# Kernel tuning notes

Hardware: AMD Instinct MI355X
Metric: run time of the kernel (lower is better)

Reference implementation:

```python
import jax, jax.numpy as jnp
import numpy as np

IMG = 1536
STRIDES = [8, 16, 32, 64, 128]
SCALES = np.array([2.0 ** 0, 2.0 ** (1.0 / 3.0), 2.0 ** (2.0 / 3.0)])
RATIOS = np.array([0.5, 1.0, 2.0])
THRESHOLD = 0.5
IOU_THRESHOLD = 0.5
N_KEEP = 1000  # fixed candidate budget for jit-compatible NMS


def make_anchors():
    """Multi-level RetinaNet-style anchors in (x1, y1, x2, y2), [A, 4]."""
    all_boxes = []
    for s in STRIDES:
        base = 4.0 * s
        fs = IMG // s
        areas = (base * SCALES) ** 2
        ws, hs = [], []
        for r in RATIOS:
            ws.append(np.sqrt(areas / r))
            hs.append(np.sqrt(areas * r))
        ws = np.concatenate(ws)  # [9]
        hs = np.concatenate(hs)
        cx = (np.arange(fs) + 0.5) * s
        cy = (np.arange(fs) + 0.5) * s
        cxg, cyg = np.meshgrid(cx, cy)
        cxg = cxg.reshape(-1, 1)
        cyg = cyg.reshape(-1, 1)
        boxes = np.stack([cxg - ws / 2, cyg - hs / 2, cxg + ws / 2, cyg + hs / 2], axis=-1)
        all_boxes.append(boxes.reshape(-1, 4))
    return np.concatenate(all_boxes, axis=0).astype(np.float32)


def setup_inputs() -> dict:
    key = jax.random.key(0)
    k1, k2 = jax.random.split(key)
    anchors = jnp.asarray(make_anchors())  # [441936, 4]
    A = anchors.shape[0]
    cla = jax.random.uniform(k1, (1, A, 80), dtype=jnp.float32)  # sigmoid-like class scores
    reg = 0.1 * jax.random.normal(k2, (1, A, 4), dtype=jnp.float32)  # box deltas
    return {"cla": cla, "reg": reg, "anchors": anchors, "height": IMG, "width": IMG}


def decode_box(anchors, deltas):
    wa = anchors[:, 2] - anchors[:, 0]
    ha = anchors[:, 3] - anchors[:, 1]
    cxa = anchors[:, 0] + 0.5 * wa
    cya = anchors[:, 1] + 0.5 * ha
    cx = cxa + deltas[:, 0] * wa
    cy = cya + deltas[:, 1] * ha
    w = wa * jnp.exp(deltas[:, 2])
    h = ha * jnp.exp(deltas[:, 3])
    return jnp.stack([cx - 0.5 * w, cy - 0.5 * h, cx + 0.5 * w, cy + 0.5 * h], axis=-1)


def iou_matrix(b):
    x1 = jnp.maximum(b[:, None, 0], b[None, :, 0])
    y1 = jnp.maximum(b[:, None, 1], b[None, :, 1])
    x2 = jnp.minimum(b[:, None, 2], b[None, :, 2])
    y2 = jnp.minimum(b[:, None, 3], b[None, :, 3])
    inter = jnp.clip(x2 - x1, 0.0) * jnp.clip(y2 - y1, 0.0)
    area = jnp.clip(b[:, 2] - b[:, 0], 0.0) * jnp.clip(b[:, 3] - b[:, 1], 0.0)
    union = area[:, None] + area[None, :] - inter
    return inter / jnp.maximum(union, 1e-8)


def reference(cla, reg, anchors, height, width):
    # decode + clip (clipbox)
    boxes = decode_box(anchors, reg[0])  # [A, 4]
    boxes = jnp.stack([
        jnp.clip(boxes[:, 0], 0.0, width - 1.0),
        jnp.clip(boxes[:, 1], 0.0, height - 1.0),
        jnp.clip(boxes[:, 2], 0.0, width - 1.0),
        jnp.clip(boxes[:, 3], 0.0, height - 1.0),
    ], axis=-1)
    # per-anchor best class score (torch.max over dim=2)
    scores_all = jnp.max(cla[0], axis=1)  # [A]
    # fixed-size candidate set replaces data-dependent boolean masking
    top_scores, idx = jax.lax.top_k(scores_all, N_KEEP)
    cand_boxes = boxes[idx]            # [N, 4]
    cand_cla = cla[0][idx]             # [N, C]
    valid = top_scores > THRESHOLD     # score thresholding
    iou = iou_matrix(cand_boxes)       # [N, N]

    def body(i, keep):
        suppressed = jnp.any(keep & (iou[i] > IOU_THRESHOLD))
        return keep.at[i].set(valid[i] & ~suppressed)

    keep = jax.lax.fori_loop(0, N_KEEP, body, jnp.zeros((N_KEEP,), dtype=bool))

    nms_scores = jnp.where(keep, jnp.max(cand_cla, axis=1), 0.0)
    nms_class = jnp.where(keep, jnp.argmax(cand_cla, axis=1), -1)
    nms_boxes = jnp.where(keep[:, None], cand_boxes, 0.0)
    return nms_scores, nms_class, nms_boxes
```

## Files before the change

### kernel.cpp

```cpp
#include <hip/hip_runtime.h>
#include <stdint.h>


#define NK 1000
#define CAP 2048
#define NCLS 80
#define NW 16
typedef unsigned long long ull;

static inline __device__ unsigned fkey(float f) {
  unsigned u = __float_as_uint(f);
  return (u & 0x80000000u) ? ~u : (u | 0x80000000u);
}
static inline __device__ float fkey_inv(unsigned k) {
  unsigned u = (k & 0x80000000u) ? (k & 0x7fffffffu) : ~k;
  return __uint_as_float(u);
}

__device__ __forceinline__ void scan_select(const unsigned* __restrict__ gh, int nbins,
                                            unsigned k, unsigned* s_sum, unsigned* s_res,
                                            unsigned& digit, unsigned& cum_above) {
  int t = threadIdx.x;
  int chunk = nbins >> 8;
  int base = t * chunk;
  unsigned s = 0;
  for (int b = 0; b < chunk; ++b) s += gh[base + b];
  s_sum[t] = s;
  __syncthreads();
  unsigned ca = 0;
  for (int u = t + 1; u < 256; ++u) ca += s_sum[u];
  if (ca < k && ca + s >= k) {
    unsigned cum = ca;
    for (int b = chunk - 1; b >= 0; --b) {
      unsigned c = gh[base + b];
      if (cum + c >= k) { s_res[0] = (unsigned)(base + b); s_res[1] = cum; break; }
      cum += c;
    }
  }
  __syncthreads();
  digit = s_res[0];
  cum_above = s_res[1];
  __syncthreads();
}

__global__ __launch_bounds__(256) void k_score(const float* __restrict__ cla,
                                               unsigned* __restrict__ keys,
                                               unsigned* __restrict__ hist0, int A) {
  __shared__ unsigned lh[4096];
  int t = threadIdx.x;
  for (int i = t; i < 4096; i += 256) lh[i] = 0u;
  __syncthreads();
  const int lane = t & 63, wib = t >> 6;
  const int gwave = blockIdx.x * 4 + wib, nwaves = gridDim.x * 4;
  const int q = lane >> 2, sub = lane & 3;
  const int ntask = (A + 15) >> 4;
  for (int task = gwave; task < ntask; task += nwaves) {
    int a = task * 16 + q;
    float m = -3.402823466e38f;
    if (a < A) {
      const float4* p = (const float4*)(cla + (size_t)a * NCLS);
#pragma unroll
      for (int j = 0; j < 5; ++j) {
        float4 v = p[sub + j * 4];
        m = fmaxf(m, fmaxf(fmaxf(v.x, v.y), fmaxf(v.z, v.w)));
      }
    }
    m = fmaxf(m, __shfl_xor(m, 1, 64));
    m = fmaxf(m, __shfl_xor(m, 2, 64));
    if (sub == 0 && a < A) {
      unsigned key = fkey(m);
      keys[a] = key;
      atomicAdd(&lh[key >> 20], 1u);
    }
  }
  __syncthreads();
  for (int i = t; i < 4096; i += 256) {
    unsigned c = lh[i];
    if (c) atomicAdd(&hist0[i], c);
  }
}

__global__ __launch_bounds__(256) void k_hist1(const unsigned* __restrict__ keys,
                                               const unsigned* __restrict__ hist0,
                                               unsigned* __restrict__ hist1, int A) {
  __shared__ unsigned lh[4096];
  __shared__ unsigned s_sum[256];
  __shared__ unsigned s_res[2];
  int t = threadIdx.x;
  unsigned d0, ca;
  scan_select(hist0, 4096, NK, s_sum, s_res, d0, ca);
  for (int i = t; i < 4096; i += 256) lh[i] = 0u;
  __syncthreads();
  int tid = blockIdx.x * 256 + t, nthr = gridDim.x * 256;
  for (int a = tid; a < A; a += nthr) {
    unsigned key = keys[a];
    if ((key >> 20) == d0) atomicAdd(&lh[(key >> 8) & 0xFFFu], 1u);
  }
  __syncthreads();
  for (int i = t; i < 4096; i += 256) {
    unsigned c = lh[i];
    if (c) atomicAdd(&hist1[i], c);
  }
}

__global__ __launch_bounds__(256) void k_hist2(const unsigned* __restrict__ keys,
                                               const unsigned* __restrict__ hist0,
                                               const unsigned* __restrict__ hist1,
                                               unsigned* __restrict__ hist2, int A) {
  __shared__ unsigned lh[256];
  __shared__ unsigned s_sum[256];
  __shared__ unsigned s_res[2];
  int t = threadIdx.x;
  unsigned k_rem = NK, d0, d1, ca;
  scan_select(hist0, 4096, k_rem, s_sum, s_res, d0, ca);
  k_rem -= ca;
  scan_select(hist1, 4096, k_rem, s_sum, s_res, d1, ca);
  unsigned pref24 = (d0 << 12) | d1;
  lh[t] = 0u;
  __syncthreads();
  int tid = blockIdx.x * 256 + t, nthr = gridDim.x * 256;
  for (int a = tid; a < A; a += nthr) {
    unsigned key = keys[a];
    if ((key >> 8) == pref24) atomicAdd(&lh[key & 0xFFu], 1u);
  }
  __syncthreads();
  unsigned c = lh[t];
  if (c) atomicAdd(&hist2[t], c);
}

__global__ __launch_bounds__(256) void k_gather(const unsigned* __restrict__ keys,
                                                const unsigned* __restrict__ hist0,
                                                const unsigned* __restrict__ hist1,
                                                const unsigned* __restrict__ hist2,
                                                unsigned* __restrict__ cand_count,
                                                ull* __restrict__ cand_keys, int A) {
  __shared__ unsigned s_sum[256];
  __shared__ unsigned s_res[2];
  __shared__ ull lbuf[1024];
  __shared__ unsigned lcnt;
  __shared__ unsigned gbase;
  int t = threadIdx.x;
  unsigned k_rem = NK, d0, d1, d2, ca;
  scan_select(hist0, 4096, k_rem, s_sum, s_res, d0, ca);
  k_rem -= ca;
  scan_select(hist1, 4096, k_rem, s_sum, s_res, d1, ca);
  k_rem -= ca;
  scan_select(hist2, 256, k_rem, s_sum, s_res, d2, ca);
  const unsigned T = (((d0 << 12) | d1) << 8) | d2;
  if (t == 0) lcnt = 0u;
  __syncthreads();
  int tid = blockIdx.x * 256 + t, nthr = gridDim.x * 256;
  for (int a = tid; a < A; a += nthr) {
    unsigned key = keys[a];
    if (key >= T) {
      unsigned pos = atomicAdd(&lcnt, 1u);
      if (pos < 1024)
        lbuf[pos] = ((ull)key << 32) | (ull)(~(unsigned)a);
    }
  }
  __syncthreads();
  if (t == 0) gbase = (lcnt > 0) ? atomicAdd(cand_count, lcnt) : 0u;
  __syncthreads();
  unsigned n = lcnt < 1024u ? lcnt : 1024u;
  for (unsigned i = t; i < n; i += 256) {
    unsigned pos = gbase + i;
    if (pos < CAP) cand_keys[pos] = lbuf[i];
  }
}

__global__ __launch_bounds__(256) void k_rankdec(
    const float* __restrict__ cla, const float* __restrict__ reg,
    const float* __restrict__ anchors, const int* __restrict__ hp,
    const int* __restrict__ wp, const ull* __restrict__ cand_keys,
    float4* __restrict__ cand_box, float* __restrict__ cand_area,
    float* __restrict__ cand_score, int* __restrict__ cand_cls,
    int* __restrict__ cand_valid) {
  __shared__ ull skeys[CAP];
  int t = threadIdx.x;
  for (int i = t; i < CAP; i += 256) skeys[i] = cand_keys[i];
  __syncthreads();
  int c = blockIdx.x * 256 + t;
  ull ck = skeys[c];
  if (ck == 0ull) return;
  unsigned cnt = 0;
  const ulonglong2* sk2 = (const ulonglong2*)skeys;
#pragma unroll 4
  for (int j = 0; j < CAP / 2; ++j) {
    ulonglong2 v = sk2[j];
    cnt += (v.x > ck) ? 1u : 0u;
    cnt += (v.y > ck) ? 1u : 0u;
  }
  if (cnt >= NK) return;
  int rank = (int)cnt;
  unsigned a = ~(unsigned)(ck & 0xFFFFFFFFull);
  float score = fkey_inv((unsigned)(ck >> 32));
  float W1 = (float)wp[0] - 1.0f;
  float H1 = (float)hp[0] - 1.0f;
  float4 dd = ((const float4*)reg)[a];
  float4 an = ((const float4*)anchors)[a];
  float wa = an.z - an.x, ha = an.w - an.y;
  float cxa = an.x + 0.5f * wa, cya = an.y + 0.5f * ha;
  float cx = cxa + dd.x * wa, cy = cya + dd.y * ha;
  float w = wa * expf(dd.z), h = ha * expf(dd.w);
  float x1 = fminf(fmaxf(cx - 0.5f * w, 0.0f), W1);
  float y1 = fminf(fmaxf(cy - 0.5f * h, 0.0f), H1);
  float x2 = fminf(fmaxf(cx + 0.5f * w, 0.0f), W1);
  float y2 = fminf(fmaxf(cy + 0.5f * h, 0.0f), H1);
  cand_box[rank] = make_float4(x1, y1, x2, y2);
  cand_area[rank] = fmaxf(x2 - x1, 0.0f) * fmaxf(y2 - y1, 0.0f);
  cand_score[rank] = score;
  cand_valid[rank] = (score > 0.5f) ? 1 : 0;
  const float* row = cla + (size_t)a * NCLS;
  float m = -3.402823466e38f;
  int ci = 0;
#pragma unroll
  for (int j = 0; j < NCLS; ++j) {
    float v = row[j];
    if (v > m) { m = v; ci = j; }
  }
  cand_cls[rank] = ci;
}

__global__ __launch_bounds__(256) void k_supmat(const float4* __restrict__ cand_box,
                                                const float* __restrict__ cand_area,
                                                ull* __restrict__ sup) {
  __shared__ float4 bx[NK];
  __shared__ float ar[NK];
  int t = threadIdx.x;
  for (int i = t; i < NK; i += 256) {
    bx[i] = cand_box[i];
    ar[i] = cand_area[i];
  }
  __syncthreads();
  int g = blockIdx.x * 256 + t;
  int i = g >> 4, w = g & 15;
  if (i >= NK) return;
  float4 bi = bx[i];
  float ai = ar[i];
  ull bits = 0ull;
  int j0 = w * 64;
  int jend = (j0 + 64 < NK) ? (j0 + 64) : NK;
  for (int j = j0; j < jend; ++j) {
    float4 bj = bx[j];
    float xx1 = fmaxf(bi.x, bj.x), yy1 = fmaxf(bi.y, bj.y);
    float xx2 = fminf(bi.z, bj.z), yy2 = fminf(bi.w, bj.w);
    float inter = fmaxf(xx2 - xx1, 0.0f) * fmaxf(yy2 - yy1, 0.0f);
    float uni = ai + ar[j] - inter;
    float iou = inter / fmaxf(uni, 1e-8f);
    if (iou > 0.5f) bits |= (1ull << (j - j0));
  }
  sup[(size_t)i * NW + w] = bits;
}

__global__ __launch_bounds__(1024) void k_resolve(const ull* __restrict__ sup,
                                                  const int* __restrict__ cand_valid,
                                                  const float* __restrict__ cand_score,
                                                  const int* __restrict__ cand_cls,
                                                  const float4* __restrict__ cand_box,
                                                  float* __restrict__ out) {
  __shared__ ull keep_sh[NW];
  int t = threadIdx.x;
  if (t < 64) {
    int lane = t;
    ull keepw[NW];
#pragma unroll
    for (int c = 0; c < NW; ++c) {
      int row = c * 64 + lane;
      ull rw[NW];
      int vld = 0;
      if (row < NK) {
#pragma unroll
        for (int w = 0; w < NW; ++w) rw[w] = sup[(size_t)row * NW + w];
        vld = cand_valid[row];
      } else {
#pragma unroll
        for (int w = 0; w < NW; ++w) rw[w] = 0ull;
      }
      ull prev = 0ull;
#pragma unroll
      for (int w = 0; w < NW; ++w)
        if (w < c) prev |= rw[w] & keepw[w];
      int flags = (vld ? 2 : 0) | ((prev != 0ull) ? 1 : 0);
      unsigned Llo = (unsigned)rw[c];
      unsigned Lhi = (unsigned)(rw[c] >> 32);
      ull kept = 0ull;
      for (int b = 0; b < 64; ++b) {
        int fb = __shfl(flags, b, 64);
        unsigned lo = (unsigned)__shfl((int)Llo, b, 64);
        unsigned hi = (unsigned)__shfl((int)Lhi, b, 64);
        ull Lb = ((ull)hi << 32) | (ull)lo;
        bool kp = ((fb & 2) != 0) && ((fb & 1) == 0) && ((Lb & kept) == 0ull);
        kept |= ((ull)(kp ? 1u : 0u)) << b;
      }
      keepw[c] = kept;
    }
    if (lane == 0) {
#pragma unroll
      for (int w = 0; w < NW; ++w) keep_sh[w] = keepw[w];
    }
  }
  __syncthreads();
  for (int i = t; i < NK; i += 1024) {
    bool kp = (keep_sh[i >> 6] >> (i & 63)) & 1ull;
    out[i] = kp ? cand_score[i] : 0.0f;
    out[NK + i] = kp ? (float)cand_cls[i] : -1.0f;
    float4 b = cand_box[i];
    ((float4*)(out + 2 * NK))[i] = kp ? b : make_float4(0.f, 0.f, 0.f, 0.f);
  }
}

extern "C" void kernel_launch(void* const* d_in, const int* in_sizes, int n_in,
                              void* d_out, int out_size, void* d_ws, size_t ws_size,
                              hipStream_t stream) {
  const float* cla = (const float*)d_in[0];
  const float* reg = (const float*)d_in[1];
  const float* anchors = (const float*)d_in[2];
  const int* hp = (const int*)d_in[3];
  const int* wp = (const int*)d_in[4];
  float* out = (float*)d_out;
  int A = in_sizes[2] / 4;

  char* ws = (char*)d_ws;
  size_t off = 0;
  auto carve = [&](size_t bytes) -> void* {
    void* p = ws + off;
    off += bytes;
    off = (off + 255) & ~(size_t)255;
    return p;
  };
  unsigned* keys = (unsigned*)carve((size_t)A * 4);
  char* zbase = ws + off;
  unsigned* hist0 = (unsigned*)carve(4096 * 4);
  unsigned* hist1 = (unsigned*)carve(4096 * 4);
  unsigned* hist2 = (unsigned*)carve(256 * 4);
  unsigned* cand_count = (unsigned*)carve(4);
  ull* cand_keys = (ull*)carve(CAP * 8);
  size_t zbytes = (size_t)((ws + off) - zbase);
  float4* cand_box = (float4*)carve(1024 * 16);
  float* cand_area = (float*)carve(1024 * 4);
  float* cand_score = (float*)carve(1024 * 4);
  int* cand_cls = (int*)carve(1024 * 4);
  int* cand_valid = (int*)carve(1024 * 4);
  ull* sup = (ull*)carve((size_t)1024 * NW * 8);
  (void)ws_size;
  (void)n_in;
  (void)out_size;

  hipMemsetAsync(zbase, 0, zbytes, stream);
  k_score<<<1024, 256, 0, stream>>>(cla, keys, hist0, A);
  k_hist1<<<512, 256, 0, stream>>>(keys, hist0, hist1, A);
  k_hist2<<<512, 256, 0, stream>>>(keys, hist0, hist1, hist2, A);
  k_gather<<<512, 256, 0, stream>>>(keys, hist0, hist1, hist2, cand_count, cand_keys, A);
  k_rankdec<<<8, 256, 0, stream>>>(cla, reg, anchors, hp, wp, cand_keys, cand_box,
                                   cand_area, cand_score, cand_cls, cand_valid);
  k_supmat<<<63, 256, 0, stream>>>(cand_box, cand_area, sup);
  k_resolve<<<1, 1024, 0, stream>>>(sup, cand_valid, cand_score, cand_cls, cand_box, out);
}
```

Baseline: 359.2 us.

## Merge radix-select passes via 20-bit leaf histogram and fuse suppression with resolve

```diff
diff --git a/kernel.cpp b/kernel.cpp
--- a/kernel.cpp
+++ b/kernel.cpp
@@ -22,6 +22,7 @@
                                             unsigned& digit, unsigned& cum_above) {
   int t = threadIdx.x;
   int chunk = nbins >> 8;
+  if (chunk < 1) chunk = 1;
   int base = t * chunk;
   unsigned s = 0;
   for (int b = 0; b < chunk; ++b) s += gh[base + b];
@@ -45,9 +46,16 @@
 
 __global__ __launch_bounds__(256) void k_score(const float* __restrict__ cla,
                                                unsigned* __restrict__ keys,
-                                               unsigned* __restrict__ hist0, int A) {
+                                               unsigned* __restrict__ hist0,
+                                               uint4* __restrict__ zreg, int nz4,
+                                               int A) {
   __shared__ unsigned lh[4096];
   int t = threadIdx.x;
+  {
+    const uint4 z = make_uint4(0u, 0u, 0u, 0u);
+    int stride = gridDim.x * 256;
+    for (int i = blockIdx.x * 256 + t; i < nz4; i += stride) zreg[i] = z;
+  }
   for (int i = t; i < 4096; i += 256) lh[i] = 0u;
   __syncthreads();
   const int lane = t & 63, wib = t >> 6;
@@ -82,7 +90,8 @@
 
 __global__ __launch_bounds__(256) void k_hist1(const unsigned* __restrict__ keys,
                                                const unsigned* __restrict__ hist0,
-                                               unsigned* __restrict__ hist1, int A) {
+                                               unsigned* __restrict__ leaf,
+                                               unsigned* __restrict__ summary, int A) {
   __shared__ unsigned lh[4096];
   __shared__ unsigned s_sum[256];
   __shared__ unsigned s_res[2];
@@ -94,45 +103,24 @@
   int tid = blockIdx.x * 256 + t, nthr = gridDim.x * 256;
   for (int a = tid; a < A; a += nthr) {
     unsigned key = keys[a];
-    if ((key >> 20) == d0) atomicAdd(&lh[(key >> 8) & 0xFFFu], 1u);
+    if ((key >> 20) == d0) {
+      unsigned low = key & 0xFFFFFu;
+      atomicAdd(&leaf[low], 1u);
+      atomicAdd(&lh[low >> 8], 1u);
+    }
   }
   __syncthreads();
   for (int i = t; i < 4096; i += 256) {
     unsigned c = lh[i];
-    if (c) atomicAdd(&hist1[i], c);
-  }
-}
-
-__global__ __launch_bounds__(256) void k_hist2(const unsigned* __restrict__ keys,
-                                               const unsigned* __restrict__ hist0,
-                                               const unsigned* __restrict__ hist1,
-                                               unsigned* __restrict__ hist2, int A) {
-  __shared__ unsigned lh[256];
-  __shared__ unsigned s_sum[256];
-  __shared__ unsigned s_res[2];
-  int t = threadIdx.x;
-  unsigned k_rem = NK, d0, d1, ca;
-  scan_select(hist0, 4096, k_rem, s_sum, s_res, d0, ca);
-  k_rem -= ca;
-  scan_select(hist1, 4096, k_rem, s_sum, s_res, d1, ca);
-  unsigned pref24 = (d0 << 12) | d1;
-  lh[t] = 0u;
-  __syncthreads();
-  int tid = blockIdx.x * 256 + t, nthr = gridDim.x * 256;
-  for (int a = tid; a < A; a += nthr) {
-    unsigned key = keys[a];
-    if ((key >> 8) == pref24) atomicAdd(&lh[key & 0xFFu], 1u);
-  }
-  __syncthreads();
-  unsigned c = lh[t];
-  if (c) atomicAdd(&hist2[t], c);
+    if (c) atomicAdd(&summary[i], c);
+  }
 }
 
 __global__ __launch_bounds__(256) void k_gather(const unsigned* __restrict__ keys,
                                                 const unsigned* __restrict__ hist0,
-                                                const unsigned* __restrict__ hist1,
-                                                const unsigned* __restrict__ hist2,
-                                                unsigned* __restrict__ cand_count,
+                                                const unsigned* __restrict__ leaf,
+                                                const unsigned* __restrict__ summary,
+                                                unsigned* __restrict__ meta,
                                                 ull* __restrict__ cand_keys, int A) {
   __shared__ unsigned s_sum[256];
   __shared__ unsigned s_res[2];
@@ -140,13 +128,13 @@
   __shared__ unsigned lcnt;
   __shared__ unsigned gbase;
   int t = threadIdx.x;
-  unsigned k_rem = NK, d0, d1, d2, ca;
+  unsigned k_rem = NK, d0, g, b, ca;
   scan_select(hist0, 4096, k_rem, s_sum, s_res, d0, ca);
   k_rem -= ca;
-  scan_select(hist1, 4096, k_rem, s_sum, s_res, d1, ca);
+  scan_select(summary, 4096, k_rem, s_sum, s_res, g, ca);
   k_rem -= ca;
-  scan_select(hist2, 256, k_rem, s_sum, s_res, d2, ca);
-  const unsigned T = (((d0 << 12) | d1) << 8) | d2;
+  scan_select(leaf + (size_t)g * 256, 256, k_rem, s_sum, s_res, b, ca);
+  const unsigned T = (d0 << 20) | (g << 8) | b;
   if (t == 0) lcnt = 0u;
   __syncthreads();
   int tid = blockIdx.x * 256 + t, nthr = gridDim.x * 256;
@@ -159,7 +147,7 @@
     }
   }
   __syncthreads();
-  if (t == 0) gbase = (lcnt > 0) ? atomicAdd(cand_count, lcnt) : 0u;
+  if (t == 0) gbase = (lcnt > 0) ? atomicAdd(&meta[0], lcnt) : 0u;
   __syncthreads();
   unsigned n = lcnt < 1024u ? lcnt : 1024u;
   for (unsigned i = t; i < n; i += 256) {
@@ -221,45 +209,53 @@
   cand_cls[rank] = ci;
 }
 
-__global__ __launch_bounds__(256) void k_supmat(const float4* __restrict__ cand_box,
+__global__ __launch_bounds__(256) void k_supres(const float4* __restrict__ cand_box,
                                                 const float* __restrict__ cand_area,
-                                                ull* __restrict__ sup) {
+                                                const int* __restrict__ cand_valid,
+                                                const float* __restrict__ cand_score,
+                                                const int* __restrict__ cand_cls,
+                                                ull* __restrict__ sup,
+                                                unsigned* __restrict__ meta,
+                                                float* __restrict__ out) {
   __shared__ float4 bx[NK];
   __shared__ float ar[NK];
+  __shared__ ull keep_sh[NW];
+  __shared__ int s_last;
   int t = threadIdx.x;
   for (int i = t; i < NK; i += 256) {
     bx[i] = cand_box[i];
     ar[i] = cand_area[i];
   }
   __syncthreads();
-  int g = blockIdx.x * 256 + t;
-  int i = g >> 4, w = g & 15;
-  if (i >= NK) return;
-  float4 bi = bx[i];
-  float ai = ar[i];
-  ull bits = 0ull;
-  int j0 = w * 64;
-  int jend = (j0 + 64 < NK) ? (j0 + 64) : NK;
-  for (int j = j0; j < jend; ++j) {
-    float4 bj = bx[j];
-    float xx1 = fmaxf(bi.x, bj.x), yy1 = fmaxf(bi.y, bj.y);
-    float xx2 = fminf(bi.z, bj.z), yy2 = fminf(bi.w, bj.w);
-    float inter = fmaxf(xx2 - xx1, 0.0f) * fmaxf(yy2 - yy1, 0.0f);
-    float uni = ai + ar[j] - inter;
-    float iou = inter / fmaxf(uni, 1e-8f);
-    if (iou > 0.5f) bits |= (1ull << (j - j0));
-  }
-  sup[(size_t)i * NW + w] = bits;
-}
-
-__global__ __launch_bounds__(1024) void k_resolve(const ull* __restrict__ sup,
-                                                  const int* __restrict__ cand_valid,
-                                                  const float* __restrict__ cand_score,
-                                                  const int* __restrict__ cand_cls,
-                                                  const float4* __restrict__ cand_box,
-                                                  float* __restrict__ out) {
-  __shared__ ull keep_sh[NW];
-  int t = threadIdx.x;
+  int gidx = blockIdx.x * 256 + t;
+  int i = gidx >> 4, w = gidx & 15;
+  if (i < NK) {
+    float4 bi = bx[i];
+    float ai = ar[i];
+    ull bits = 0ull;
+    int j0 = w * 64;
+    int jend = (j0 + 64 < NK) ? (j0 + 64) : NK;
+    for (int j = j0; j < jend; ++j) {
+      float4 bj = bx[j];
+      float xx1 = fmaxf(bi.x, bj.x), yy1 = fmaxf(bi.y, bj.y);
+      float xx2 = fminf(bi.z, bj.z), yy2 = fminf(bi.w, bj.w);
+      float inter = fmaxf(xx2 - xx1, 0.0f) * fmaxf(yy2 - yy1, 0.0f);
+      float uni = ai + ar[j] - inter;
+      float iou = inter / fmaxf(uni, 1e-8f);
+      if (iou > 0.5f) bits |= (1ull << (j - j0));
+    }
+    sup[(size_t)i * NW + w] = bits;
+  }
+  __threadfence();
+  __syncthreads();
+  if (t == 0) {
+    unsigned done = __hip_atomic_fetch_add(&meta[1], 1u, __ATOMIC_ACQ_REL,
+                                           __HIP_MEMORY_SCOPE_AGENT);
+    s_last = (done == gridDim.x - 1) ? 1 : 0;
+  }
+  __syncthreads();
+  if (!s_last) return;
+  __threadfence();
   if (t < 64) {
     int lane = t;
     ull keepw[NW];
@@ -270,16 +266,18 @@
       int vld = 0;
       if (row < NK) {
 #pragma unroll
-        for (int w = 0; w < NW; ++w) rw[w] = sup[(size_t)row * NW + w];
+        for (int w2 = 0; w2 < NW; ++w2)
+          rw[w2] = __hip_atomic_load(&sup[(size_t)row * NW + w2], __ATOMIC_RELAXED,
+                                     __HIP_MEMORY_SCOPE_AGENT);
         vld = cand_valid[row];
       } else {
 #pragma unroll
-        for (int w = 0; w < NW; ++w) rw[w] = 0ull;
+        for (int w2 = 0; w2 < NW; ++w2) rw[w2] = 0ull;
       }
       ull prev = 0ull;
 #pragma unroll
-      for (int w = 0; w < NW; ++w)
-        if (w < c) prev |= rw[w] & keepw[w];
+      for (int w2 = 0; w2 < NW; ++w2)
+        if (w2 < c) prev |= rw[w2] & keepw[w2];
       int flags = (vld ? 2 : 0) | ((prev != 0ull) ? 1 : 0);
       unsigned Llo = (unsigned)rw[c];
       unsigned Lhi = (unsigned)(rw[c] >> 32);
@@ -296,16 +294,16 @@
     }
     if (lane == 0) {
 #pragma unroll
-      for (int w = 0; w < NW; ++w) keep_sh[w] = keepw[w];
-    }
-  }
-  __syncthreads();
-  for (int i = t; i < NK; i += 1024) {
-    bool kp = (keep_sh[i >> 6] >> (i & 63)) & 1ull;
-    out[i] = kp ? cand_score[i] : 0.0f;
-    out[NK + i] = kp ? (float)cand_cls[i] : -1.0f;
-    float4 b = cand_box[i];
-    ((float4*)(out + 2 * NK))[i] = kp ? b : make_float4(0.f, 0.f, 0.f, 0.f);
+      for (int w2 = 0; w2 < NW; ++w2) keep_sh[w2] = keepw[w2];
+    }
+  }
+  __syncthreads();
+  for (int i2 = t; i2 < NK; i2 += 256) {
+    bool kp = (keep_sh[i2 >> 6] >> (i2 & 63)) & 1ull;
+    out[i2] = kp ? cand_score[i2] : 0.0f;
+    out[NK + i2] = kp ? (float)cand_cls[i2] : -1.0f;
+    float4 bo = cand_box[i2];
+    ((float4*)(out + 2 * NK))[i2] = kp ? bo : make_float4(0.f, 0.f, 0.f, 0.f);
   }
 }
 
@@ -329,13 +327,14 @@
     return p;
   };
   unsigned* keys = (unsigned*)carve((size_t)A * 4);
+  unsigned* hist0 = (unsigned*)carve(4096 * 4);
   char* zbase = ws + off;
-  unsigned* hist0 = (unsigned*)carve(4096 * 4);
-  unsigned* hist1 = (unsigned*)carve(4096 * 4);
-  unsigned* hist2 = (unsigned*)carve(256 * 4);
-  unsigned* cand_count = (unsigned*)carve(4);
+  unsigned* leaf = (unsigned*)carve((size_t)(1 << 20) * 4);
+  unsigned* summary = (unsigned*)carve(4096 * 4);
+  unsigned* meta = (unsigned*)carve(2 * 4);
   ull* cand_keys = (ull*)carve(CAP * 8);
   size_t zbytes = (size_t)((ws + off) - zbase);
+  int nz4 = (int)(zbytes / 16);
   float4* cand_box = (float4*)carve(1024 * 16);
   float* cand_area = (float*)carve(1024 * 4);
   float* cand_score = (float*)carve(1024 * 4);
@@ -346,13 +345,12 @@
   (void)n_in;
   (void)out_size;
 
-  hipMemsetAsync(zbase, 0, zbytes, stream);
-  k_score<<<1024, 256, 0, stream>>>(cla, keys, hist0, A);
-  k_hist1<<<512, 256, 0, stream>>>(keys, hist0, hist1, A);
-  k_hist2<<<512, 256, 0, stream>>>(keys, hist0, hist1, hist2, A);
-  k_gather<<<512, 256, 0, stream>>>(keys, hist0, hist1, hist2, cand_count, cand_keys, A);
+  hipMemsetAsync(hist0, 0, 4096 * 4, stream);
+  k_score<<<1024, 256, 0, stream>>>(cla, keys, hist0, (uint4*)zbase, nz4, A);
+  k_hist1<<<512, 256, 0, stream>>>(keys, hist0, leaf, summary, A);
+  k_gather<<<512, 256, 0, stream>>>(keys, hist0, leaf, summary, meta, cand_keys, A);
   k_rankdec<<<8, 256, 0, stream>>>(cla, reg, anchors, hp, wp, cand_keys, cand_box,
                                    cand_area, cand_score, cand_cls, cand_valid);
-  k_supmat<<<63, 256, 0, stream>>>(cand_box, cand_area, sup);
-  k_resolve<<<1, 1024, 0, stream>>>(sup, cand_valid, cand_score, cand_cls, cand_box, out);
-}
+  k_supres<<<63, 256, 0, stream>>>(cand_box, cand_area, cand_valid, cand_score,
+                                   cand_cls, sup, meta, out);
+}
```

Measured after the change: 379.0 us. +5.5%, slower.
